# Kernel optimization log

Hardware: AMD Instinct MI355X
Metric: run time of the kernel (lower is better)

## Reference

```python
import jax, jax.numpy as jnp
import numpy as np

ALPHA = 1.0  # set_privacy(True)


def setup_inputs() -> dict:
    key = jax.random.key(0)
    k1, k2, k3, k4, k5, k6 = jax.random.split(key, 6)
    B, S, IN, OUT = 2, 1024, 4096, 11008
    NNZ = 2250000
    x = jax.random.normal(k1, (B, S, IN), dtype=jnp.float32)
    scales = jax.random.uniform(k2, (OUT,), dtype=jnp.float32)  # positive per-row scales
    ortho_vals = jax.random.normal(k3, (NNZ,), dtype=jnp.float32)
    base_packed = jax.random.randint(k4, (OUT, IN // 2), 0, 256, dtype=jnp.int32)
    ortho_rows = jnp.sort(jax.random.randint(k5, (NNZ,), 0, OUT, dtype=jnp.int32))
    ortho_cols = jax.random.randint(k6, (NNZ,), 0, IN, dtype=jnp.int32)
    return {"x": x, "scales": scales, "ortho_vals": ortho_vals,
            "base_packed": base_packed, "ortho_rows": ortho_rows, "ortho_cols": ortho_cols}


def _dequant_weight(base_packed, scales):
    OUT, HALF = base_packed.shape
    low = base_packed & 0xF          # packed column 2j  -> original column 2j
    high = (base_packed >> 4) & 0xF  # packed column 2j  -> original column 2j+1
    # interleave low/high nibbles back to [OUT, IN]
    w_off = jnp.stack([low, high], axis=-1).reshape(OUT, 2 * HALF)
    return (w_off.astype(jnp.float32) - 8.0) * scales[:, None]


def reference(x, scales, ortho_vals, base_packed, ortho_rows, ortho_cols):
    OUT = base_packed.shape[0]
    IN = base_packed.shape[1] * 2
    w_base = _dequant_weight(base_packed, scales)  # [OUT, IN] fp32
    w_sparse = jnp.zeros((OUT, IN), dtype=jnp.float32).at[ortho_rows, ortho_cols].add(
        ortho_vals.astype(jnp.float32))
    w = w_base + ALPHA * w_sparse
    x_flat = x.reshape(-1, IN).astype(jnp.float32)
    out = x_flat @ w.T  # [tokens, OUT]
    return out.reshape(x.shape[:-1] + (OUT,)).astype(x.dtype)
```

## Files before the change

### kernel.cpp

```cpp
#include <hip/hip_runtime.h>
#include <stdint.h>

#define ALPHA 1.0f

typedef int i32x4 __attribute__((ext_vector_type(4)));

typedef __attribute__((address_space(3))) void lds_void_t;
typedef const __attribute__((address_space(1))) void global_void_t;

__device__ __forceinline__ void async16(const void* g, void* l) {
    __builtin_amdgcn_global_load_lds((global_void_t*)g, (lds_void_t*)l, 16, 0, 0);
}

__device__ __forceinline__ signed char q8(float v, float inv) {
    float f = fminf(fmaxf(v * inv, -127.f), 127.f);
    return (signed char)__float2int_rn(f);
}

__global__ __launch_bounds__(256) void prep_kernel(
    const float* __restrict__ x, const int* __restrict__ rows,
    int* __restrict__ rstart, int* __restrict__ rend,
    signed char* __restrict__ X8, float* __restrict__ sx, int M, int nnz) {
    const int b = blockIdx.x;
    if (b < M) {
        __shared__ float red[4];
        const int t = threadIdx.x;
        const float4* xr = (const float4*)(x + (size_t)b * 4096);
        float4 v[4];
        float mx = 0.f;
#pragma unroll
        for (int i = 0; i < 4; i++) {
            v[i] = xr[t * 4 + i];
            mx = fmaxf(mx, fmaxf(fmaxf(fabsf(v[i].x), fabsf(v[i].y)),
                                 fmaxf(fabsf(v[i].z), fabsf(v[i].w))));
        }
#pragma unroll
        for (int o = 32; o > 0; o >>= 1) mx = fmaxf(mx, __shfl_xor(mx, o));
        if ((t & 63) == 0) red[t >> 6] = mx;
        __syncthreads();
        mx = fmaxf(fmaxf(red[0], red[1]), fmaxf(red[2], red[3]));
        mx = fmaxf(mx, 1e-20f);
        if (t == 0) sx[b] = mx / 127.f;
        const float inv = 127.f / mx;
        union { signed char c[16]; int4 w; } u;
#pragma unroll
        for (int i = 0; i < 4; i++) {
            u.c[i * 4 + 0] = q8(v[i].x, inv);
            u.c[i * 4 + 1] = q8(v[i].y, inv);
            u.c[i * 4 + 2] = q8(v[i].z, inv);
            u.c[i * 4 + 3] = q8(v[i].w, inv);
        }
        ((int4*)(X8 + (size_t)b * 4096))[t] = u.w;
    } else {
        int i = (b - M) * 256 + threadIdx.x;
        if (i < nnz) {
            int r = rows[i];
            if (i == 0 || rows[i - 1] != r) rstart[r] = i;
            if (i == nnz - 1 || rows[i + 1] != r) rend[r] = i + 1;
        }
    }
}

__global__ __launch_bounds__(256) void build_w8_kernel(
    const int* __restrict__ packed, const float* __restrict__ scales,
    const float* __restrict__ vals, const int* __restrict__ cols,
    const int* __restrict__ rstart, const int* __restrict__ rend,
    signed char* __restrict__ W8, float* __restrict__ sw) {
    __shared__ float acc[4096];
    __shared__ float red[4];
    const int r = blockIdx.x;
    const int t = threadIdx.x;
    const int4* prow = (const int4*)(packed + (size_t)r * 2048);
    const float s = scales[r];

    int4 p0 = prow[t], p1 = prow[t + 256];
#pragma unroll
    for (int h = 0; h < 2; h++) {
        int4 p = h ? p1 : p0;
        int base = 8 * (t + 256 * h);
        int pv[4] = {p.x, p.y, p.z, p.w};
#pragma unroll
        for (int q = 0; q < 4; q++) {
            acc[base + 2 * q]     = (float)((pv[q] & 0xF) - 8) * s;
            acc[base + 2 * q + 1] = (float)(((pv[q] >> 4) & 0xF) - 8) * s;
        }
    }
    __syncthreads();

    const int lo = rstart[r], hi = rend[r];
    for (int i = lo + t; i < hi; i += 256)
        atomicAdd(&acc[cols[i]], vals[i] * ALPHA);
    __syncthreads();

    float4 f[4];
    float mx = 0.f;
#pragma unroll
    for (int i = 0; i < 4; i++) {
        f[i] = ((const float4*)acc)[t * 4 + i];
        mx = fmaxf(mx, fmaxf(fmaxf(fabsf(f[i].x), fabsf(f[i].y)),
                             fmaxf(fabsf(f[i].z), fabsf(f[i].w))));
    }
#pragma unroll
    for (int o = 32; o > 0; o >>= 1) mx = fmaxf(mx, __shfl_xor(mx, o));
    if ((t & 63) == 0) red[t >> 6] = mx;
    __syncthreads();
    mx = fmaxf(fmaxf(red[0], red[1]), fmaxf(red[2], red[3]));
    mx = fmaxf(mx, 1e-20f);
    if (t == 0) sw[r] = mx / 127.f;
    const float inv = 127.f / mx;

    union { signed char c[16]; int4 w; } u;
#pragma unroll
    for (int i = 0; i < 4; i++) {
        u.c[i * 4 + 0] = q8(f[i].x, inv);
        u.c[i * 4 + 1] = q8(f[i].y, inv);
        u.c[i * 4 + 2] = q8(f[i].z, inv);
        u.c[i * 4 + 3] = q8(f[i].w, inv);
    }
    ((int4*)(W8 + (size_t)r * 4096))[t] = u.w;
}

__global__ __launch_bounds__(512) void gemm_kernel(
    const signed char* __restrict__ Xq,
    const signed char* __restrict__ Wq,
    const float* __restrict__ sx,
    const float* __restrict__ sw,
    float* __restrict__ C,
    int M, int N, int K) {
    __shared__ __align__(16) signed char smem[3 * 49152];

    const int tid  = threadIdx.x;
    const int wid  = tid >> 6;
    const int lane = tid & 63;
    const int wr = wid >> 2;
    const int wc = wid & 3;

    const int nwg = gridDim.x;
    const int bid = blockIdx.x;
    const int qc = nwg >> 3, rr = nwg & 7;
    const int xcd = bid & 7, loc = bid >> 3;
    const int swz = (xcd < rr ? xcd * (qc + 1) : rr * (qc + 1) + (xcd - rr) * qc) + loc;
    const int tm = M >> 7;
    const int mt = swz % tm;
    const int nt = swz / tm;
    const int m0 = mt << 7;
    const int n0 = nt << 8;

    const int sr = tid >> 3;
    const int sc = ((tid & 7) ^ (sr & 7)) << 4;
    const int lw0 = wid << 10;
    const int lw1 = 8192 + (wid << 10);

    const signed char* Ax  = Xq + (size_t)m0 * K;
    const signed char* Bw0 = Wq + (size_t)n0 * K;
    const signed char* Bw1 = Wq + (size_t)(n0 + 128) * K;

#define STAGE(gbase, ldsbase) do {                                         \
        async16((gbase) + (size_t)sr * K + sc, (ldsbase) + lw0);           \
        async16((gbase) + (size_t)(sr + 64) * K + sc, (ldsbase) + lw1);    \
    } while (0)

    const int fm = lane & 15;
    const int slot0 = ((lane >> 4) ^ (lane & 7)) << 4;
    const int slot1 = slot0 ^ 64;
    const int arow_base = wr * 64;
    const int brow_base = wc * 64;

    i32x4 acc[4][4];
#pragma unroll
    for (int i = 0; i < 4; i++)
#pragma unroll
        for (int j = 0; j < 4; j++) acc[i][j] = (i32x4){0, 0, 0, 0};

    const int NT = K >> 7;

    STAGE(Ax,        smem);
    STAGE(Bw0,       smem + 16384);
    STAGE(Bw1,       smem + 32768);
    STAGE(Ax  + 128, smem + 49152);
    STAGE(Bw0 + 128, smem + 49152 + 16384);
    STAGE(Bw1 + 128, smem + 49152 + 32768);
    asm volatile("s_waitcnt vmcnt(6)" ::: "memory");
    __builtin_amdgcn_s_barrier();
    __builtin_amdgcn_sched_barrier(0);

    int cur = 0;
    for (int it = 0; it < NT; ++it) {
        signed char* Ab = smem + cur * 49152;
        signed char* Bb = Ab + 16384;
        int pb = cur + 2; if (pb >= 3) pb -= 3;
        signed char* PA   = smem + pb * 49152;
        signed char* PBlo = PA + 16384;
        signed char* PBhi = PA + 32768;
        const bool pref = (it + 2 < NT);
        const int kc = (it + 2) << 7;

        i32x4 bfr[4];
#pragma unroll
        for (int p = 0; p < 4; ++p) {
            const int sl = (p >> 1) ? slot1 : slot0;
            const int mib = (p & 1) << 1;
            i32x4 a0 = *(const i32x4*)(Ab + (arow_base + (mib + 0) * 16 + fm) * 128 + sl);
            i32x4 a1 = *(const i32x4*)(Ab + (arow_base + (mib + 1) * 16 + fm) * 128 + sl);
            if ((p & 1) == 0) {
#pragma unroll
                for (int nj = 0; nj < 4; ++nj)
                    bfr[nj] = *(const i32x4*)(Bb + (brow_base + nj * 16 + fm) * 128 + sl);
            }
            if (pref) {
                if (p == 0)      STAGE(Ax  + kc, PA);
                else if (p == 1) STAGE(Bw0 + kc, PBlo);
                else if (p == 2) STAGE(Bw1 + kc, PBhi);
            }
            __builtin_amdgcn_s_barrier();
            asm volatile("s_waitcnt lgkmcnt(0)" ::: "memory");
            __builtin_amdgcn_sched_barrier(0);
            __builtin_amdgcn_s_setprio(1);
#pragma unroll
            for (int nj = 0; nj < 4; ++nj) {
                acc[mib + 0][nj] = __builtin_amdgcn_mfma_i32_16x16x64_i8(
                    a0, bfr[nj], acc[mib + 0][nj], 0, 0, 0);
                acc[mib + 1][nj] = __builtin_amdgcn_mfma_i32_16x16x64_i8(
                    a1, bfr[nj], acc[mib + 1][nj], 0, 0, 0);
            }
            __builtin_amdgcn_s_setprio(0);
            if (p == 3) {
                if (it + 2 < NT)       { asm volatile("s_waitcnt vmcnt(6)" ::: "memory"); }
                else if (it + 2 == NT) { asm volatile("s_waitcnt vmcnt(0)" ::: "memory"); }
            }
            __builtin_amdgcn_s_barrier();
            if (p == 3) __builtin_amdgcn_sched_barrier(0);
        }
        cur += 1; if (cur == 3) cur = 0;
    }
#undef STAGE

    const int cr = (lane >> 4) << 2;
    const int cc = lane & 15;
#pragma unroll
    for (int mi = 0; mi < 4; ++mi) {
        const int row0 = m0 + wr * 64 + mi * 16 + cr;
        float sxv[4];
#pragma unroll
        for (int r = 0; r < 4; ++r) sxv[r] = sx[row0 + r];
#pragma unroll
        for (int nj = 0; nj < 4; ++nj) {
            const int col = n0 + wc * 64 + nj * 16 + cc;
            const float swc = sw[col];
            float* cp = C + (size_t)row0 * N + col;
#pragma unroll
            for (int r = 0; r < 4; ++r)
                cp[(size_t)r * N] = (float)acc[mi][nj][r] * sxv[r] * swc;
        }
    }
}

extern "C" void kernel_launch(void* const* d_in, const int* in_sizes, int n_in,
                              void* d_out, int out_size, void* d_ws, size_t ws_size,
                              hipStream_t stream) {
    const float* x      = (const float*)d_in[0];
    const float* scales = (const float*)d_in[1];
    const float* vals   = (const float*)d_in[2];
    const int* packed   = (const int*)d_in[3];
    const int* rows     = (const int*)d_in[4];
    const int* cols     = (const int*)d_in[5];
    float* out          = (float*)d_out;

    const int OUT  = in_sizes[1];
    const int HALF = in_sizes[3] / OUT;
    const int IN   = HALF * 2;
    const int M    = in_sizes[0] / IN;
    const int NNZ  = in_sizes[2];

    signed char* W8 = (signed char*)d_ws;
    signed char* X8 = W8 + (size_t)OUT * IN;
    float* sx   = (float*)(X8 + (size_t)M * IN);
    float* sw   = sx + M;
    int* rstart = (int*)(sw + OUT);
    int* rend   = rstart + OUT;

    const int boundsBlocks = (NNZ + 255) / 256;
    prep_kernel<<<M + boundsBlocks, 256, 0, stream>>>(x, rows, rstart, rend,
                                                      X8, sx, M, NNZ);
    build_w8_kernel<<<OUT, 256, 0, stream>>>(packed, scales, vals, cols,
                                             rstart, rend, W8, sw);
    const int nwg = (M / 128) * (OUT / 256);
    gemm_kernel<<<nwg, 512, 0, stream>>>(X8, W8, sx, sw, out, M, OUT, IN);
}
```

Measured before the change: 321.5 us.

## Restructure int8 GEMM main loop to software-pipeline LDS reads with one barrier per tile

```diff
diff --git a/kernel.cpp b/kernel.cpp
--- a/kernel.cpp
+++ b/kernel.cpp
@@ -166,6 +166,24 @@
     const int arow_base = wr * 64;
     const int brow_base = wc * 64;
 
+#define LDA(buf, mi, sl) \
+    (*(const i32x4*)((buf) + (size_t)(arow_base + (mi) * 16 + fm) * 128 + (sl)))
+#define LDB(buf, nj, sl) \
+    (*(const i32x4*)((buf) + 16384 + (size_t)(brow_base + (nj) * 16 + fm) * 128 + (sl)))
+
+#define MFMA8(m0i, m1i, aX, aY, B0, B1, B2, B3) do {                        \
+        __builtin_amdgcn_s_setprio(1);                                      \
+        acc[m0i][0] = __builtin_amdgcn_mfma_i32_16x16x64_i8(aX, B0, acc[m0i][0], 0, 0, 0); \
+        acc[m1i][0] = __builtin_amdgcn_mfma_i32_16x16x64_i8(aY, B0, acc[m1i][0], 0, 0, 0); \
+        acc[m0i][1] = __builtin_amdgcn_mfma_i32_16x16x64_i8(aX, B1, acc[m0i][1], 0, 0, 0); \
+        acc[m1i][1] = __builtin_amdgcn_mfma_i32_16x16x64_i8(aY, B1, acc[m1i][1], 0, 0, 0); \
+        acc[m0i][2] = __builtin_amdgcn_mfma_i32_16x16x64_i8(aX, B2, acc[m0i][2], 0, 0, 0); \
+        acc[m1i][2] = __builtin_amdgcn_mfma_i32_16x16x64_i8(aY, B2, acc[m1i][2], 0, 0, 0); \
+        acc[m0i][3] = __builtin_amdgcn_mfma_i32_16x16x64_i8(aX, B3, acc[m0i][3], 0, 0, 0); \
+        acc[m1i][3] = __builtin_amdgcn_mfma_i32_16x16x64_i8(aY, B3, acc[m1i][3], 0, 0, 0); \
+        __builtin_amdgcn_s_setprio(0);                                      \
+    } while (0)
+
     i32x4 acc[4][4];
 #pragma unroll
     for (int i = 0; i < 4; i++)
@@ -187,53 +205,40 @@
     int cur = 0;
     for (int it = 0; it < NT; ++it) {
         signed char* Ab = smem + cur * 49152;
-        signed char* Bb = Ab + 16384;
         int pb = cur + 2; if (pb >= 3) pb -= 3;
-        signed char* PA   = smem + pb * 49152;
-        signed char* PBlo = PA + 16384;
-        signed char* PBhi = PA + 32768;
+        signed char* PA = smem + pb * 49152;
         const bool pref = (it + 2 < NT);
         const int kc = (it + 2) << 7;
 
-        i32x4 bfr[4];
-#pragma unroll
-        for (int p = 0; p < 4; ++p) {
-            const int sl = (p >> 1) ? slot1 : slot0;
-            const int mib = (p & 1) << 1;
-            i32x4 a0 = *(const i32x4*)(Ab + (arow_base + (mib + 0) * 16 + fm) * 128 + sl);
-            i32x4 a1 = *(const i32x4*)(Ab + (arow_base + (mib + 1) * 16 + fm) * 128 + sl);
-            if ((p & 1) == 0) {
-#pragma unroll
-                for (int nj = 0; nj < 4; ++nj)
-                    bfr[nj] = *(const i32x4*)(Bb + (brow_base + nj * 16 + fm) * 128 + sl);
-            }
-            if (pref) {
-                if (p == 0)      STAGE(Ax  + kc, PA);
-                else if (p == 1) STAGE(Bw0 + kc, PBlo);
-                else if (p == 2) STAGE(Bw1 + kc, PBhi);
-            }
-            __builtin_amdgcn_s_barrier();
-            asm volatile("s_waitcnt lgkmcnt(0)" ::: "memory");
-            __builtin_amdgcn_sched_barrier(0);
-            __builtin_amdgcn_s_setprio(1);
-#pragma unroll
-            for (int nj = 0; nj < 4; ++nj) {
-                acc[mib + 0][nj] = __builtin_amdgcn_mfma_i32_16x16x64_i8(
-                    a0, bfr[nj], acc[mib + 0][nj], 0, 0, 0);
-                acc[mib + 1][nj] = __builtin_amdgcn_mfma_i32_16x16x64_i8(
-                    a1, bfr[nj], acc[mib + 1][nj], 0, 0, 0);
-            }
-            __builtin_amdgcn_s_setprio(0);
-            if (p == 3) {
-                if (it + 2 < NT)       { asm volatile("s_waitcnt vmcnt(6)" ::: "memory"); }
-                else if (it + 2 == NT) { asm volatile("s_waitcnt vmcnt(0)" ::: "memory"); }
-            }
-            __builtin_amdgcn_s_barrier();
-            if (p == 3) __builtin_amdgcn_sched_barrier(0);
-        }
+        i32x4 a0  = LDA(Ab, 0, slot0), a1  = LDA(Ab, 1, slot0);
+        i32x4 bA0 = LDB(Ab, 0, slot0), bA1 = LDB(Ab, 1, slot0),
+              bA2 = LDB(Ab, 2, slot0), bA3 = LDB(Ab, 3, slot0);
+        i32x4 na0 = LDA(Ab, 2, slot0), na1 = LDA(Ab, 3, slot0);
+        if (pref) STAGE(Ax + kc, PA);
+        MFMA8(0, 1, a0, a1, bA0, bA1, bA2, bA3);
+
+        i32x4 bB0 = LDB(Ab, 0, slot1), bB1 = LDB(Ab, 1, slot1),
+              bB2 = LDB(Ab, 2, slot1), bB3 = LDB(Ab, 3, slot1);
+        i32x4 ma0 = LDA(Ab, 0, slot1), ma1 = LDA(Ab, 1, slot1);
+        if (pref) STAGE(Bw0 + kc, PA + 16384);
+        MFMA8(2, 3, na0, na1, bA0, bA1, bA2, bA3);
+
+        i32x4 pa2 = LDA(Ab, 2, slot1), pa3 = LDA(Ab, 3, slot1);
+        if (pref) STAGE(Bw1 + kc, PA + 32768);
+        MFMA8(0, 1, ma0, ma1, bB0, bB1, bB2, bB3);
+
+        if (it + 2 < NT)       { asm volatile("s_waitcnt vmcnt(6)" ::: "memory"); }
+        else if (it + 2 == NT) { asm volatile("s_waitcnt vmcnt(0)" ::: "memory"); }
+        MFMA8(2, 3, pa2, pa3, bB0, bB1, bB2, bB3);
+
+        __builtin_amdgcn_s_barrier();
+        __builtin_amdgcn_sched_barrier(0);
         cur += 1; if (cur == 3) cur = 0;
     }
 #undef STAGE
+#undef LDA
+#undef LDB
+#undef MFMA8
 
     const int cr = (lane >> 4) << 2;
     const int cc = lane & 15;
```

After: 314.0 us. -2.3%, faster.
